# Performance work log

Measured on AMD Instinct MI355X. Metric: run time of the kernel, lower is better.

The kernel has to match this reference:

```python
import jax, jax.numpy as jnp
import numpy as np

N_STATE = 64
D_MODEL = 512
BATCH = 4
SEQ_LEN = 2048


def setup_inputs() -> dict:
    key = jax.random.key(0)
    k1, k2, k3, k4 = jax.random.split(key, 4)
    # Parameters, matching torch init: A = diag(rand(N) * A_scale), B/C = rand(N)
    A = jnp.diag(jax.random.uniform(k1, (N_STATE,), dtype=jnp.float32))  # (N, N), full matrix param
    Bvec = jax.random.uniform(k2, (N_STATE,), dtype=jnp.float32)  # (N,)
    Cvec = jax.random.uniform(k3, (N_STATE,), dtype=jnp.float32)  # (N,)
    u = jax.random.normal(k4, (BATCH, D_MODEL, SEQ_LEN), dtype=jnp.float32)  # (B, H=d_model, L)
    return {"u": u, "A": A, "Bvec": Bvec, "Cvec": Cvec, "L": SEQ_LEN}


def reference(u, A, Bvec, Cvec, L):
    # Faithful translation of the recurrent branch of NonSelectiveSSMKernel.forward:
    #   h_l = A @ h_{l-1} + B (outer) u[:, :, l];   y[:, :, l] = C . h_l
    # expressed as a lax.scan over the time axis (A is a full NxN matrix parameter).
    Bsz, d, _ = u.shape
    N = A.shape[0]
    u_t = jnp.transpose(u, (2, 0, 1))  # (L, B, d)
    h0 = jnp.zeros((Bsz, N, d), dtype=u.dtype)

    def step(h, u_l):  # h: (B, N, d), u_l: (B, d)
        h = jnp.einsum('ij,bjd->bid', A, h) + Bvec[None, :, None] * u_l[:, None, :]
        y_l = jnp.einsum('i,bid->bd', Cvec, h)
        return h, y_l

    _, y = jax.lax.scan(step, h0, u_t)  # y: (L, B, d)
    return jnp.transpose(y, (1, 2, 0))  # (B, d, L)
```

## Files before the change

### kernel.cpp

```cpp
#include <hip/hip_runtime.h>


#define N_STATE 64
#define D_MODEL 512
#define BATCH   4
#define SEQ     2048
#define NCH     (BATCH * D_MODEL)
#define WAVES   4
#define TSTEP   64
#define TSTRIDE 68

__global__ __launch_bounds__(WAVES * 64, 1)
void NonSelectiveSSMKernel_scan(const float* __restrict__ u,
                                const float* __restrict__ A,
                                const float* __restrict__ Bv,
                                const float* __restrict__ Cv,
                                float* __restrict__ y)
{
    __shared__ float tile[WAVES][TSTEP][TSTRIDE];

    const int wave = threadIdx.x >> 6;
    const int lane = threadIdx.x & 63;
    const int ch   = blockIdx.x * WAVES + wave;

    const float* __restrict__ uc = u + (size_t)ch * SEQ;
    float* __restrict__       yc = y + (size_t)ch * SEQ;

    const float a  = A[lane * (N_STATE + 1)];
    const float cb = Bv[lane] * Cv[lane];

    float g = 0.0f;
    float (*tl)[TSTRIDE] = tile[wave];

    for (int t0 = 0; t0 < SEQ; t0 += TSTEP) {
        float ur = uc[t0 + lane];

        #pragma unroll
        for (int t = 0; t < TSTEP; ++t) {
            int   ui   = __builtin_amdgcn_readlane(__float_as_int(ur), t);
            float uval = __int_as_float(ui);
            g = a * g + cb * uval;
            tl[t][lane] = g;
        }

        float ysum = 0.0f;
        #pragma unroll
        for (int i = 0; i < N_STATE; i += 4) {
            float4 v = *reinterpret_cast<const float4*>(&tl[lane][i]);
            ysum += (v.x + v.y) + (v.z + v.w);
        }
        yc[t0 + lane] = ysum;
    }
}

extern "C" void kernel_launch(void* const* d_in, const int* in_sizes, int n_in,
                              void* d_out, int out_size, void* d_ws, size_t ws_size,
                              hipStream_t stream)
{
    const float* u  = (const float*)d_in[0];
    const float* A  = (const float*)d_in[1];
    const float* Bv = (const float*)d_in[2];
    const float* Cv = (const float*)d_in[3];
    float*       y  = (float*)d_out;

    dim3 grid(NCH / WAVES);
    dim3 block(WAVES * 64);
    NonSelectiveSSMKernel_scan<<<grid, block, 0, stream>>>(u, A, Bv, Cv, y);
}
```

Before: 59.29 us.

## Split sequence into four chunks with a three-pass chunked scan

Replaces the single sequential scan per channel with three kernels. The first computes each chunk's final state, the second carries states across the four chunks using a^512, and the third rescans each chunk from its carried-in state and reduces outputs in 16-step sub-tiles. This gives four times as many waves so the serial recurrence length per wave is quarter as long, at the cost of reading u twice, two extra launches and workspace traffic. The original kernel is kept as a fallback when the workspace is too small.

```diff
diff --git a/kernel.cpp b/kernel.cpp
--- a/kernel.cpp
+++ b/kernel.cpp
@@ -1,51 +1,155 @@
 #include <hip/hip_runtime.h>
 
 
-#define N_STATE 64
-#define D_MODEL 512
-#define BATCH   4
-#define SEQ     2048
-#define NCH     (BATCH * D_MODEL)
-#define WAVES   4
-#define TSTEP   64
-#define TSTRIDE 68
+#define NCH   2048
+#define LSEQ  2048
+#define NQ    4
+#define QL    512
+#define E_OFF 0
+#define M_OFF (2u*1024u*1024u)
+#define WS_NEED (4u*1024u*1024u)
 
-__global__ __launch_bounds__(WAVES * 64, 1)
-void NonSelectiveSSMKernel_scan(const float* __restrict__ u,
-                                const float* __restrict__ A,
-                                const float* __restrict__ Bv,
-                                const float* __restrict__ Cv,
-                                float* __restrict__ y)
+__global__ __launch_bounds__(256) void ssm_partial(const float* __restrict__ u,
+                                                   const float* __restrict__ A,
+                                                   const float* __restrict__ Bv,
+                                                   float* __restrict__ E)
 {
-    __shared__ float tile[WAVES][TSTEP][TSTRIDE];
+    const int lane = threadIdx.x & 63;
+    const int wv   = threadIdx.x >> 6;
+    const int widx = blockIdx.x * 4 + wv;
+    const int q    = widx & 3;
+    const int ch   = widx >> 2;
 
+    const float a = A[lane * 65];
+    const float b = Bv[lane];
+    const float* __restrict__ base = u + (size_t)ch * LSEQ + q * QL;
+
+    float ur[8];
+    #pragma unroll
+    for (int blk = 0; blk < 8; ++blk) ur[blk] = base[blk * 64 + lane];
+
+    float h = 0.f;
+    #pragma unroll
+    for (int blk = 0; blk < 8; ++blk){
+        #pragma unroll
+        for (int tt = 0; tt < 64; ++tt){
+            float uv = __int_as_float(__builtin_amdgcn_readlane(__float_as_int(ur[blk]), tt));
+            h = fmaf(a, h, b * uv);
+        }
+    }
+    E[((size_t)q * NCH + ch) * 64 + lane] = h;
+}
+
+__global__ __launch_bounds__(256) void ssm_combine(const float* __restrict__ A,
+                                                   const float* __restrict__ Cv,
+                                                   const float* __restrict__ E,
+                                                   float* __restrict__ M)
+{
+    const int tid = blockIdx.x * 256 + threadIdx.x;
+    const int i   = tid & 63;
+    const int ch  = tid >> 6;
+
+    const float a = A[i * 65];
+    float a512 = a;
+    #pragma unroll
+    for (int s = 0; s < 9; ++s) a512 *= a512;
+    const float c = Cv[i];
+
+    float S = 0.f;
+    #pragma unroll
+    for (int q = 0; q < NQ; ++q){
+        const size_t off = ((size_t)q * NCH + ch) * 64 + i;
+        M[off] = c * S;
+        S = fmaf(a512, S, E[off]);
+    }
+}
+
+__global__ __launch_bounds__(256) void ssm_scan(const float* __restrict__ u,
+                                                const float* __restrict__ A,
+                                                const float* __restrict__ Bv,
+                                                const float* __restrict__ Cv,
+                                                const float* __restrict__ M,
+                                                float* __restrict__ y)
+{
+    __shared__ float tile[4][16][68];
+
+    const int lane = threadIdx.x & 63;
+    const int wv   = threadIdx.x >> 6;
+    const int widx = blockIdx.x * 4 + wv;
+    const int q    = widx & 3;
+    const int ch   = widx >> 2;
+
+    const float a  = A[lane * 65];
+    const float cb = Bv[lane] * Cv[lane];
+    const float* __restrict__ base = u + (size_t)ch * LSEQ + q * QL;
+    float* __restrict__       yc   = y + (size_t)ch * LSEQ + q * QL;
+
+    float g = M[((size_t)q * NCH + ch) * 64 + lane];
+
+    float (*tl)[68] = tile[wv];
+    const int j    = lane & 15;
+    const int part = lane >> 4;
+
+    float ur[8];
+    #pragma unroll
+    for (int blk = 0; blk < 8; ++blk) ur[blk] = base[blk * 64 + lane];
+
+    #pragma unroll
+    for (int blk = 0; blk < 8; ++blk){
+        #pragma unroll
+        for (int sub = 0; sub < 4; ++sub){
+            #pragma unroll
+            for (int tt = 0; tt < 16; ++tt){
+                float uv = __int_as_float(
+                    __builtin_amdgcn_readlane(__float_as_int(ur[blk]), sub * 16 + tt));
+                g = fmaf(a, g, cb * uv);
+                tl[tt][lane] = g;
+            }
+            float4 v0 = *reinterpret_cast<const float4*>(&tl[j][16 * part + 0]);
+            float4 v1 = *reinterpret_cast<const float4*>(&tl[j][16 * part + 4]);
+            float4 v2 = *reinterpret_cast<const float4*>(&tl[j][16 * part + 8]);
+            float4 v3 = *reinterpret_cast<const float4*>(&tl[j][16 * part + 12]);
+            float v = ((v0.x + v0.y) + (v0.z + v0.w)) + ((v1.x + v1.y) + (v1.z + v1.w))
+                    + ((v2.x + v2.y) + (v2.z + v2.w)) + ((v3.x + v3.y) + (v3.z + v3.w));
+            v += __shfl_xor(v, 16, 64);
+            v += __shfl_xor(v, 32, 64);
+            if (lane < 16) yc[blk * 64 + sub * 16 + lane] = v;
+        }
+    }
+}
+
+__global__ __launch_bounds__(256, 1) void ssm_r1(const float* __restrict__ u,
+                                                 const float* __restrict__ A,
+                                                 const float* __restrict__ Bv,
+                                                 const float* __restrict__ Cv,
+                                                 float* __restrict__ y)
+{
+    __shared__ float tile[4][64][68];
     const int wave = threadIdx.x >> 6;
     const int lane = threadIdx.x & 63;
-    const int ch   = blockIdx.x * WAVES + wave;
+    const int ch   = blockIdx.x * 4 + wave;
 
-    const float* __restrict__ uc = u + (size_t)ch * SEQ;
-    float* __restrict__       yc = y + (size_t)ch * SEQ;
+    const float* __restrict__ uc = u + (size_t)ch * LSEQ;
+    float* __restrict__       yc = y + (size_t)ch * LSEQ;
 
-    const float a  = A[lane * (N_STATE + 1)];
+    const float a  = A[lane * 65];
     const float cb = Bv[lane] * Cv[lane];
 
     float g = 0.0f;
-    float (*tl)[TSTRIDE] = tile[wave];
+    float (*tl)[68] = tile[wave];
 
-    for (int t0 = 0; t0 < SEQ; t0 += TSTEP) {
+    for (int t0 = 0; t0 < LSEQ; t0 += 64){
         float ur = uc[t0 + lane];
-
         #pragma unroll
-        for (int t = 0; t < TSTEP; ++t) {
+        for (int t = 0; t < 64; ++t){
             int   ui   = __builtin_amdgcn_readlane(__float_as_int(ur), t);
             float uval = __int_as_float(ui);
-            g = a * g + cb * uval;
+            g = fmaf(a, g, cb * uval);
             tl[t][lane] = g;
         }
-
         float ysum = 0.0f;
         #pragma unroll
-        for (int i = 0; i < N_STATE; i += 4) {
+        for (int i = 0; i < 64; i += 4){
             float4 v = *reinterpret_cast<const float4*>(&tl[lane][i]);
             ysum += (v.x + v.y) + (v.z + v.w);
         }
@@ -61,9 +165,16 @@
     const float* A  = (const float*)d_in[1];
     const float* Bv = (const float*)d_in[2];
     const float* Cv = (const float*)d_in[3];
-    float*       y  = (float*)d_out;
+    float*       yo = (float*)d_out;
+    char*        ws = (char*)d_ws;
 
-    dim3 grid(NCH / WAVES);
-    dim3 block(WAVES * 64);
-    NonSelectiveSSMKernel_scan<<<grid, block, 0, stream>>>(u, A, Bv, Cv, y);
+    if (ws_size >= WS_NEED){
+        float* E = (float*)(ws + E_OFF);
+        float* M = (float*)(ws + M_OFF);
+        ssm_partial<<<NCH * NQ / 4, 256, 0, stream>>>(u, A, Bv, E);
+        ssm_combine<<<NCH * 64 / 256, 256, 0, stream>>>(A, Cv, E, M);
+        ssm_scan<<<NCH * NQ / 4, 256, 0, stream>>>(u, A, Bv, Cv, M, yo);
+    } else {
+        ssm_r1<<<NCH / 4, 256, 0, stream>>>(u, A, Bv, Cv, yo);
+    }
 }
```

New measurement: 70.08 us. +18.2%, slower.
